# Optimization experiments

Hardware: AMD Instinct MI355X
Metric: run time of the kernel (lower is better)

The kernel has to match this reference:

```python
import jax, jax.numpy as jnp
import numpy as np

LN_EPS = 1e-5

def _layer_norm(x, gamma, beta):
    mu = jnp.mean(x, axis=-1, keepdims=True)
    var = jnp.mean(jnp.square(x - mu), axis=-1, keepdims=True)
    return (x - mu) * jax.lax.rsqrt(var + LN_EPS) * gamma + beta


def setup_inputs() -> dict:
    key = jax.random.key(0)
    ks = jax.random.split(key, 6)
    B, V, N, T, H = 16, 32000, 50, 128, 768
    return {
        "common_voc_embed": jax.random.normal(ks[0], (V, H), dtype=jnp.float32),
        "ocr_embed": jax.random.normal(ks[1], (B, N, H), dtype=jnp.float32),
        "prev_ids": jax.random.randint(ks[2], (B, T), 0, V + N, dtype=jnp.int64),
        "cv_gamma": jnp.ones((H,), jnp.float32),
        "cv_beta": jnp.zeros((H,), jnp.float32),
        "ocr_gamma": jnp.ones((H,), jnp.float32),
        "ocr_beta": jnp.zeros((H,), jnp.float32),
        "pos_emb": jax.random.normal(ks[3], (T, H), dtype=jnp.float32),
        "type_emb": jax.random.normal(ks[4], (2, H), dtype=jnp.float32),
        "emb_gamma": jnp.ones((H,), jnp.float32),
        "emb_beta": jnp.zeros((H,), jnp.float32),
    }


def reference(common_voc_embed, ocr_embed, prev_ids, cv_gamma, cv_beta,
              ocr_gamma, ocr_beta, pos_emb, type_emb, emb_gamma, emb_beta):
    # common_voc_embed: [V, H], ocr_embed: [B, N, H], prev_ids: [B, T]
    V = common_voc_embed.shape[0]
    N = ocr_embed.shape[1]
    B, T = prev_ids.shape

    # LayerNorm both source tables (matches torch normalizing before concat)
    cv_n = _layer_norm(common_voc_embed, cv_gamma, cv_beta)   # [V, H]
    ocr_n = _layer_norm(ocr_embed, ocr_gamma, ocr_beta)        # [B, N, H]

    # Batched gather from the virtual concat([cv_n (shared), ocr_n], dim=1)
    # without materializing the [B, V+N, H] table.
    is_ocr = prev_ids >= V                                     # [B, T]
    cv_rows = cv_n[jnp.clip(prev_ids, 0, V - 1)]               # [B, T, H]
    ocr_idx = jnp.clip(prev_ids - V, 0, N - 1)                 # [B, T]
    ocr_rows = jnp.take_along_axis(ocr_n, ocr_idx[..., None], axis=1)  # [B, T, H]
    last_word_embeds = jnp.where(is_ocr[..., None], ocr_rows, cv_rows)

    # Position + token-type embeddings (type_ids = position >= vocab_size,
    # replicated faithfully from the source even though it is always 0 here)
    position_ids = jnp.arange(T, dtype=jnp.int32)              # [T]
    position_embeds = pos_emb[position_ids]                    # [T, H]
    type_ids = (position_ids >= V).astype(jnp.int32)           # [T]
    token_type_embeds = type_emb[type_ids]                     # [T, H]
    pos_type = _layer_norm(position_embeds + token_type_embeds, emb_gamma, emb_beta)
    # Dropout is identity in eval mode.
    return last_word_embeds + pos_type[None, :, :]             # [B, T, H]
```

## Files before the change

### kernel.cpp

```cpp
#include <hip/hip_runtime.h>

#define LN_EPS 1e-5f

constexpr int kH = 768;
constexpr int kBlock = 256;
constexpr int kPer = kH / kBlock;

__global__ __launch_bounds__(kBlock) void prev_embed_fused(
    const float* __restrict__ cv,
    const float* __restrict__ ocr,
    const int*   __restrict__ ids,
    const float* __restrict__ cv_g, const float* __restrict__ cv_b,
    const float* __restrict__ ocr_g, const float* __restrict__ ocr_b,
    const float* __restrict__ pos,
    const float* __restrict__ type_emb,
    const float* __restrict__ emb_g, const float* __restrict__ emb_b,
    float* __restrict__ out,
    int V, int N, int T)
{
    const int bt  = blockIdx.x;
    const int t   = bt % T;
    const int b   = bt / T;
    const int tid = threadIdx.x;

    const int id = ids[bt];
    const float* grow;
    const float* gamma;
    const float* beta;
    if (id >= V) {
        int oi = id - V;
        oi = oi < 0 ? 0 : (oi > N - 1 ? N - 1 : oi);
        grow  = ocr + ((size_t)b * N + oi) * kH;
        gamma = ocr_g; beta = ocr_b;
    } else {
        int ci = id < 0 ? 0 : (id > V - 1 ? V - 1 : id);
        grow  = cv + (size_t)ci * kH;
        gamma = cv_g; beta = cv_b;
    }
    const float* trow = type_emb + ((t >= V) ? kH : 0);
    const float* prow = pos + (size_t)t * kH;

    float x[kPer], p[kPer];
    float4 acc = make_float4(0.f, 0.f, 0.f, 0.f);
#pragma unroll
    for (int k = 0; k < kPer; ++k) {
        const int i = tid + k * kBlock;
        const float xv = grow[i];
        const float pv = prow[i] + trow[i];
        x[k] = xv; p[k] = pv;
        acc.x += xv; acc.y += xv * xv;
        acc.z += pv; acc.w += pv * pv;
    }

#pragma unroll
    for (int off = 32; off >= 1; off >>= 1) {
        acc.x += __shfl_xor(acc.x, off);
        acc.y += __shfl_xor(acc.y, off);
        acc.z += __shfl_xor(acc.z, off);
        acc.w += __shfl_xor(acc.w, off);
    }
    __shared__ float4 sred[kBlock / 64];
    const int wid = tid >> 6;
    if ((tid & 63) == 0) sred[wid] = acc;
    __syncthreads();
    float4 tot = sred[0];
#pragma unroll
    for (int w = 1; w < kBlock / 64; ++w) {
        const float4 s = sred[w];
        tot.x += s.x; tot.y += s.y; tot.z += s.z; tot.w += s.w;
    }

    const float invH = 1.0f / (float)kH;
    const float mux = tot.x * invH;
    const float rsx = rsqrtf(fmaxf(tot.y * invH - mux * mux, 0.f) + LN_EPS);
    const float mup = tot.z * invH;
    const float rsp = rsqrtf(fmaxf(tot.w * invH - mup * mup, 0.f) + LN_EPS);

    float* orow = out + (size_t)bt * kH;
#pragma unroll
    for (int k = 0; k < kPer; ++k) {
        const int i = tid + k * kBlock;
        const float xn = (x[k] - mux) * rsx * gamma[i] + beta[i];
        const float pn = (p[k] - mup) * rsp * emb_g[i] + emb_b[i];
        orow[i] = xn + pn;
    }
}

extern "C" void kernel_launch(void* const* d_in, const int* in_sizes, int n_in,
                              void* d_out, int out_size, void* d_ws, size_t ws_size,
                              hipStream_t stream) {
    const float* cv    = (const float*)d_in[0];
    const float* ocr   = (const float*)d_in[1];
    const int*   ids   = (const int*)d_in[2];
    const float* cv_g  = (const float*)d_in[3];
    const float* cv_b  = (const float*)d_in[4];
    const float* ocr_g = (const float*)d_in[5];
    const float* ocr_b = (const float*)d_in[6];
    const float* pos   = (const float*)d_in[7];
    const float* typ   = (const float*)d_in[8];
    const float* emb_g = (const float*)d_in[9];
    const float* emb_b = (const float*)d_in[10];
    float* out = (float*)d_out;

    const int H  = in_sizes[3];
    const int V  = in_sizes[0] / H;
    const int T  = in_sizes[7] / H;
    const int BT = in_sizes[2];
    const int B  = BT / T;
    const int N  = in_sizes[1] / (B * H);
    (void)out_size; (void)d_ws; (void)ws_size; (void)n_in;

    prev_embed_fused<<<BT, kBlock, 0, stream>>>(
        cv, ocr, ids, cv_g, cv_b, ocr_g, ocr_b, pos, typ, emb_g, emb_b,
        out, V, N, T);
}
```

Baseline: 143.2 us.

## Map one wavefront per row with float4 loads, dropping block-level reduction

Each 64-lane wavefront now handles a whole (b,t) row instead of a 256-thread block per row, with four rows packed per block. Loads and stores use float4 vectors. The row statistics come from wave shuffles alone, which removes the shared-memory reduction and __syncthreads. The grid shrinks by a factor of four, and the launch assumes BT is divisible by four.

```diff
diff --git a/kernel.cpp b/kernel.cpp
--- a/kernel.cpp
+++ b/kernel.cpp
@@ -2,9 +2,10 @@
 
 #define LN_EPS 1e-5f
 
-constexpr int kH = 768;
-constexpr int kBlock = 256;
-constexpr int kPer = kH / kBlock;
+constexpr int kH   = 768;
+constexpr int kRPB = 4;
+constexpr int kBlock = 64 * kRPB;
+constexpr int kVec = kH / (64 * 4);
 
 __global__ __launch_bounds__(kBlock) void prev_embed_fused(
     const float* __restrict__ cv,
@@ -18,10 +19,11 @@
     float* __restrict__ out,
     int V, int N, int T)
 {
-    const int bt  = blockIdx.x;
-    const int t   = bt % T;
-    const int b   = bt / T;
-    const int tid = threadIdx.x;
+    const int wave = threadIdx.x >> 6;
+    const int lane = threadIdx.x & 63;
+    const int bt   = blockIdx.x * kRPB + wave;
+    const int t    = bt % T;
+    const int b    = bt / T;
 
     const int id = ids[bt];
     const float* grow;
@@ -37,52 +39,56 @@
         grow  = cv + (size_t)ci * kH;
         gamma = cv_g; beta = cv_b;
     }
-    const float* trow = type_emb + ((t >= V) ? kH : 0);
-    const float* prow = pos + (size_t)t * kH;
+    const float4* grow4 = (const float4*)grow;
+    const float4* prow4 = (const float4*)(pos + (size_t)t * kH);
+    const float4* trow4 = (const float4*)(type_emb + ((t >= V) ? kH : 0));
 
-    float x[kPer], p[kPer];
-    float4 acc = make_float4(0.f, 0.f, 0.f, 0.f);
+    float4 x[kVec], p[kVec];
+    float sx = 0.f, sxx = 0.f, sp = 0.f, spp = 0.f;
 #pragma unroll
-    for (int k = 0; k < kPer; ++k) {
-        const int i = tid + k * kBlock;
-        const float xv = grow[i];
-        const float pv = prow[i] + trow[i];
+    for (int k = 0; k < kVec; ++k) {
+        const int i = lane + k * 64;
+        float4 xv = grow4[i];
+        float4 pv = prow4[i];
+        const float4 tv = trow4[i];
+        pv.x += tv.x; pv.y += tv.y; pv.z += tv.z; pv.w += tv.w;
         x[k] = xv; p[k] = pv;
-        acc.x += xv; acc.y += xv * xv;
-        acc.z += pv; acc.w += pv * pv;
+        sx  += xv.x + xv.y + xv.z + xv.w;
+        sxx += xv.x * xv.x + xv.y * xv.y + xv.z * xv.z + xv.w * xv.w;
+        sp  += pv.x + pv.y + pv.z + pv.w;
+        spp += pv.x * pv.x + pv.y * pv.y + pv.z * pv.z + pv.w * pv.w;
     }
 
 #pragma unroll
     for (int off = 32; off >= 1; off >>= 1) {
-        acc.x += __shfl_xor(acc.x, off);
-        acc.y += __shfl_xor(acc.y, off);
-        acc.z += __shfl_xor(acc.z, off);
-        acc.w += __shfl_xor(acc.w, off);
-    }
-    __shared__ float4 sred[kBlock / 64];
-    const int wid = tid >> 6;
-    if ((tid & 63) == 0) sred[wid] = acc;
-    __syncthreads();
-    float4 tot = sred[0];
-#pragma unroll
-    for (int w = 1; w < kBlock / 64; ++w) {
-        const float4 s = sred[w];
-        tot.x += s.x; tot.y += s.y; tot.z += s.z; tot.w += s.w;
+        sx  += __shfl_xor(sx,  off);
+        sxx += __shfl_xor(sxx, off);
+        sp  += __shfl_xor(sp,  off);
+        spp += __shfl_xor(spp, off);
     }
 
     const float invH = 1.0f / (float)kH;
-    const float mux = tot.x * invH;
-    const float rsx = rsqrtf(fmaxf(tot.y * invH - mux * mux, 0.f) + LN_EPS);
-    const float mup = tot.z * invH;
-    const float rsp = rsqrtf(fmaxf(tot.w * invH - mup * mup, 0.f) + LN_EPS);
+    const float mux = sx * invH;
+    const float rsx = rsqrtf(fmaxf(sxx * invH - mux * mux, 0.f) + LN_EPS);
+    const float mup = sp * invH;
+    const float rsp = rsqrtf(fmaxf(spp * invH - mup * mup, 0.f) + LN_EPS);
 
-    float* orow = out + (size_t)bt * kH;
+    const float4* g4  = (const float4*)gamma;
+    const float4* b4  = (const float4*)beta;
+    const float4* eg4 = (const float4*)emb_g;
+    const float4* eb4 = (const float4*)emb_b;
+    float4* orow4 = (float4*)(out + (size_t)bt * kH);
 #pragma unroll
-    for (int k = 0; k < kPer; ++k) {
-        const int i = tid + k * kBlock;
-        const float xn = (x[k] - mux) * rsx * gamma[i] + beta[i];
-        const float pn = (p[k] - mup) * rsp * emb_g[i] + emb_b[i];
-        orow[i] = xn + pn;
+    for (int k = 0; k < kVec; ++k) {
+        const int i = lane + k * 64;
+        const float4 gv = g4[i],  bv = b4[i];
+        const float4 ev = eg4[i], fv = eb4[i];
+        float4 o;
+        o.x = (x[k].x - mux) * rsx * gv.x + bv.x + (p[k].x - mup) * rsp * ev.x + fv.x;
+        o.y = (x[k].y - mux) * rsx * gv.y + bv.y + (p[k].y - mup) * rsp * ev.y + fv.y;
+        o.z = (x[k].z - mux) * rsx * gv.z + bv.z + (p[k].z - mup) * rsp * ev.z + fv.z;
+        o.w = (x[k].w - mux) * rsx * gv.w + bv.w + (p[k].w - mup) * rsp * ev.w + fv.w;
+        orow4[i] = o;
     }
 }
 
@@ -110,7 +116,7 @@
     const int N  = in_sizes[1] / (B * H);
     (void)out_size; (void)d_ws; (void)ws_size; (void)n_in;
 
-    prev_embed_fused<<<BT, kBlock, 0, stream>>>(
+    prev_embed_fused<<<BT / kRPB, kBlock, 0, stream>>>(
         cv, ocr, ids, cv_g, cv_b, ocr_g, ocr_b, pos, typ, emb_g, emb_b,
         out, V, N, T);
 }
```

New measurement: 143.0 us. No clear change (-0.1%).
